# Kernel tuning notes

Measured on AMD Instinct MI355X. Metric: run time of the kernel, lower is better.

The kernel has to match this reference:

```python
import jax, jax.numpy as jnp
import numpy as np

NUM_EMBEDDINGS = 1024
EMBEDDING_DIM = 64


def setup_inputs() -> dict:
    key = jax.random.key(0)
    k1, k2 = jax.random.split(key)
    x = jax.random.normal(k1, (32, 64, 32, 32), dtype=jnp.float32)
    # embeddings initialized uniform(-1/K, 1/K) as in the torch module
    codebook = jax.random.uniform(
        k2, (NUM_EMBEDDINGS, EMBEDDING_DIM), dtype=jnp.float32,
        minval=-1.0 / NUM_EMBEDDINGS, maxval=1.0 / NUM_EMBEDDINGS)
    return {"x": x, "codebook": codebook}


def reference(x, codebook):
    # x: [B, D, H, W] -> [B, H, W, D]
    xp = jnp.transpose(x, (0, 2, 3, 1))
    B, H, W, D = xp.shape
    K = codebook.shape[0]
    xf = xp.reshape(-1, D)  # [N, D]
    # squared L2 distances via expansion (argmin identical to torch.norm argmin)
    x2 = jnp.sum(xf * xf, axis=1, keepdims=True)          # [N, 1]
    c2 = jnp.sum(codebook * codebook, axis=1)             # [K]
    d2 = x2 - 2.0 * (xf @ codebook.T) + c2[None, :]       # [N, K]
    idx = jnp.argmin(d2, axis=1)                          # [N]
    encodings = jax.nn.one_hot(idx, K, dtype=jnp.float32)  # [N, K]
    quantized = codebook[idx]                             # [N, D] == encodings @ codebook
    quantized = quantized.reshape(B, H, W, D).transpose(0, 3, 1, 2)
    return encodings, quantized
```

## Files before the change

kernel.cpp:

```cpp
#include <hip/hip_runtime.h>

#define N_PIX    32768
#define DIM      64
#define K_CODES  1024
#define NCHUNK   4
#define CHUNK    256
#define BPIX     128
#define CS_STR   260


__global__ __launch_bounds__(256) void c2_kernel(const float* __restrict__ cb,
                                                 float* __restrict__ c2) {
    int k = blockIdx.x * 256 + threadIdx.x;
    if (k >= K_CODES) return;
    const float* row = cb + k * DIM;
    float a0 = 0.f, a1 = 0.f, a2 = 0.f, a3 = 0.f;
#pragma unroll
    for (int d = 0; d < DIM; d += 4) {
        a0 = fmaf(row[d + 0], row[d + 0], a0);
        a1 = fmaf(row[d + 1], row[d + 1], a1);
        a2 = fmaf(row[d + 2], row[d + 2], a2);
        a3 = fmaf(row[d + 3], row[d + 3], a3);
    }
    c2[k] = (a0 + a1) + (a2 + a3);
}

__global__ __launch_bounds__(512, 2) void argmin_tile(const float* __restrict__ x,
                                                      const float* __restrict__ cb,
                                                      const float* __restrict__ c2,
                                                      int* __restrict__ idx,
                                                      float* __restrict__ quant) {
    __shared__ alignas(16) float xs[DIM * BPIX];
    __shared__ alignas(16) float cs[DIM * CS_STR];
    __shared__ float  xn[BPIX];
    __shared__ float2 red[4][BPIX];

    const int t      = threadIdx.x;
    const int blk    = blockIdx.x;
    const int p_base = blk * BPIX;
    const int bb     = p_base >> 10;
    const int hw0    = p_base & 1023;

    const float4* x4  = reinterpret_cast<const float4*>(x);
    const float4* cb4 = reinterpret_cast<const float4*>(cb);

#pragma unroll
    for (int i = 0; i < 4; ++i) {
        int fidx = i * 512 + t;
        int d = fidx >> 5, p4 = fidx & 31;
        float4 v = x4[(size_t)bb * 16384 + (size_t)d * 256 + (hw0 >> 2) + p4];
        *reinterpret_cast<float4*>(&xs[d * BPIX + p4 * 4]) = v;
    }
    __syncthreads();

    if (t < BPIX) {
        float s0 = 0.f, s1 = 0.f, s2 = 0.f, s3 = 0.f;
#pragma unroll
        for (int d = 0; d < DIM; d += 4) {
            float v0 = xs[(d + 0) * BPIX + t];
            float v1 = xs[(d + 1) * BPIX + t];
            float v2 = xs[(d + 2) * BPIX + t];
            float v3 = xs[(d + 3) * BPIX + t];
            s0 = fmaf(v0, v0, s0);
            s1 = fmaf(v1, v1, s1);
            s2 = fmaf(v2, v2, s2);
            s3 = fmaf(v3, v3, s3);
        }
        xn[t] = (s0 + s1) + (s2 + s3);
    }

    const int lane = t & 63, w = t >> 6;
    const int wy = lane >> 3, wx = lane & 7;
    const int wr = w >> 2,    wc = w & 3;
    const int pl0 = wr * 64 + wy * 8;
    const int kl0 = wc * 64 + wx * 8;

    float bv[8]; int bk[8]; float xnr[8];
#pragma unroll
    for (int i = 0; i < 8; ++i) { bv[i] = 1e30f; bk[i] = 0; }

    float4 creg[8];
#pragma unroll
    for (int i = 0; i < 8; ++i) {
        int fidx = i * 512 + t; int k = fidx & 255, dq = fidx >> 8;
        creg[i] = cb4[(size_t)k * 16 + dq];
    }
    __syncthreads();

#pragma unroll
    for (int i = 0; i < 8; ++i) xnr[i] = xn[pl0 + i];

    for (int c = 0; c < NCHUNK; ++c) {
#pragma unroll
        for (int i = 0; i < 8; ++i) {
            int fidx = i * 512 + t; int k = fidx & 255, dq = fidx >> 8;
            cs[(4 * dq + 0) * CS_STR + k] = creg[i].x;
            cs[(4 * dq + 1) * CS_STR + k] = creg[i].y;
            cs[(4 * dq + 2) * CS_STR + k] = creg[i].z;
            cs[(4 * dq + 3) * CS_STR + k] = creg[i].w;
        }
        if (c + 1 < NCHUNK) {
#pragma unroll
            for (int i = 0; i < 8; ++i) {
                int fidx = i * 512 + t; int k = fidx & 255, dq = fidx >> 8;
                creg[i] = cb4[(size_t)((c + 1) * CHUNK + k) * 16 + dq];
            }
        }
        __syncthreads();

        float acc[8][8];
#pragma unroll
        for (int i = 0; i < 8; ++i)
#pragma unroll
            for (int j = 0; j < 8; ++j) acc[i][j] = 0.f;

#pragma unroll 4
        for (int d = 0; d < DIM; ++d) {
            const float* xr = &xs[d * BPIX + pl0];
            const float* cr = &cs[d * CS_STR + kl0];
            float4 xlo = *reinterpret_cast<const float4*>(xr);
            float4 xhi = *reinterpret_cast<const float4*>(xr + 4);
            float4 clo = *reinterpret_cast<const float4*>(cr);
            float4 chi = *reinterpret_cast<const float4*>(cr + 4);
#define ROW(i, xi) \
            acc[i][0] = fmaf(xi, clo.x, acc[i][0]); \
            acc[i][1] = fmaf(xi, clo.y, acc[i][1]); \
            acc[i][2] = fmaf(xi, clo.z, acc[i][2]); \
            acc[i][3] = fmaf(xi, clo.w, acc[i][3]); \
            acc[i][4] = fmaf(xi, chi.x, acc[i][4]); \
            acc[i][5] = fmaf(xi, chi.y, acc[i][5]); \
            acc[i][6] = fmaf(xi, chi.z, acc[i][6]); \
            acc[i][7] = fmaf(xi, chi.w, acc[i][7]);
            ROW(0, xlo.x) ROW(1, xlo.y) ROW(2, xlo.z) ROW(3, xlo.w)
            ROW(4, xhi.x) ROW(5, xhi.y) ROW(6, xhi.z) ROW(7, xhi.w)
#undef ROW
        }

        float4 c2lo = *reinterpret_cast<const float4*>(&c2[c * CHUNK + kl0]);
        float4 c2hi = *reinterpret_cast<const float4*>(&c2[c * CHUNK + kl0 + 4]);
        float c2a[8] = {c2lo.x, c2lo.y, c2lo.z, c2lo.w, c2hi.x, c2hi.y, c2hi.z, c2hi.w};
#pragma unroll
        for (int i = 0; i < 8; ++i) {
#pragma unroll
            for (int j = 0; j < 8; ++j) {
                int   k    = c * CHUNK + kl0 + j;
                float u    = xnr[i] - 2.0f * acc[i][j];
                float dist = u + c2a[j];
                if (dist < bv[i]) { bv[i] = dist; bk[i] = k; }
            }
        }
        __syncthreads();
    }

#pragma unroll
    for (int i = 0; i < 8; ++i) {
#pragma unroll
        for (int off = 1; off <= 4; off <<= 1) {
            float ov = __shfl_xor(bv[i], off);
            int   ok = __shfl_xor(bk[i], off);
            if (ov < bv[i] || (ov == bv[i] && ok < bk[i])) { bv[i] = ov; bk[i] = ok; }
        }
    }
    if (wx == 0) {
#pragma unroll
        for (int i = 0; i < 8; ++i)
            red[wc][pl0 + i] = make_float2(bv[i], __int_as_float(bk[i]));
    }
    __syncthreads();

    if (t < BPIX) {
        float fv = 1e30f; int fk = 0;
#pragma unroll
        for (int cc = 0; cc < 4; ++cc) {
            float2 r  = red[cc][t];
            int    rk = __float_as_int(r.y);
            if (r.x < fv || (r.x == fv && rk < fk)) { fv = r.x; fk = rk; }
        }
        idx[p_base + t] = fk;

        const float4* crow = cb4 + (size_t)fk * 16;
        float* qb = quant + (size_t)bb * (DIM * 1024) + (hw0 + t);
#pragma unroll
        for (int dq = 0; dq < 16; ++dq) {
            float4 cv = crow[dq];
            qb[(size_t)(dq * 4 + 0) << 10] = cv.x;
            qb[(size_t)(dq * 4 + 1) << 10] = cv.y;
            qb[(size_t)(dq * 4 + 2) << 10] = cv.z;
            qb[(size_t)(dq * 4 + 3) << 10] = cv.w;
        }
    }
}

__global__ __launch_bounds__(256) void enc_write(const int* __restrict__ idx,
                                                 float* __restrict__ enc) {
    const int TOT = (N_PIX / 4) * K_CODES;
    int tid = blockIdx.x * 256 + threadIdx.x;
    float4* enc4 = reinterpret_cast<float4*>(enc);
    for (int e = tid; e < TOT; e += 2048 * 256) {
        int n  = e >> 8;
        int j0 = (e & 255) << 2;
        int ir = idx[n];
        float4 v;
        v.x = (ir == j0 + 0) ? 1.0f : 0.0f;
        v.y = (ir == j0 + 1) ? 1.0f : 0.0f;
        v.z = (ir == j0 + 2) ? 1.0f : 0.0f;
        v.w = (ir == j0 + 3) ? 1.0f : 0.0f;
        enc4[e] = v;
    }
}

extern "C" void kernel_launch(void* const* d_in, const int* in_sizes, int n_in,
                              void* d_out, int out_size, void* d_ws, size_t ws_size,
                              hipStream_t stream) {
    const float* x  = (const float*)d_in[0];
    const float* cb = (const float*)d_in[1];

    float* c2  = (float*)d_ws;
    int*   idx = (int*)((char*)d_ws + 4096);

    float* enc   = (float*)d_out;
    float* quant = (float*)d_out + (size_t)N_PIX * K_CODES;

    c2_kernel<<<K_CODES / 256, 256, 0, stream>>>(cb, c2);
    argmin_tile<<<N_PIX / BPIX, 512, 0, stream>>>(x, cb, c2, idx, quant);
    enc_write<<<2048, 256, 0, stream>>>(idx, enc);
}
```

Before: 208.9 us.

## Split codebook across blocks with larger pixel tiles and separate reduce kernel

The argmin kernel now handles 256 pixels per block, and each block covers only half of the codebook, so the grid has 256 blocks. Each thread computes an 8x16 register tile instead of 8x8 to raise the ratio of FMAs to LDS reads. The unpadded codebook tile is read at strided float4 offsets. A new reduce_quant kernel merges the two half-codebook partial minima and writes the idx and quantized outputs. The trade-offs are higher register pressure from the 128 accumulators, an extra kernel launch, and a round trip through global memory for the partial results.

```diff
diff --git a/kernel.cpp b/kernel.cpp
--- a/kernel.cpp
+++ b/kernel.cpp
@@ -3,10 +3,9 @@
 #define N_PIX    32768
 #define DIM      64
 #define K_CODES  1024
-#define NCHUNK   4
+#define BPIX     256
 #define CHUNK    256
-#define BPIX     128
-#define CS_STR   260
+#define NSPLIT   2
 
 
 __global__ __launch_bounds__(256) void c2_kernel(const float* __restrict__ cb,
@@ -28,28 +27,37 @@
 __global__ __launch_bounds__(512, 2) void argmin_tile(const float* __restrict__ x,
                                                       const float* __restrict__ cb,
                                                       const float* __restrict__ c2,
-                                                      int* __restrict__ idx,
-                                                      float* __restrict__ quant) {
+                                                      float2* __restrict__ part) {
     __shared__ alignas(16) float xs[DIM * BPIX];
-    __shared__ alignas(16) float cs[DIM * CS_STR];
+    __shared__ alignas(16) float cs[DIM * CHUNK];
     __shared__ float  xn[BPIX];
-    __shared__ float2 red[4][BPIX];
+    __shared__ float2 red[2][BPIX];
 
     const int t      = threadIdx.x;
     const int blk    = blockIdx.x;
-    const int p_base = blk * BPIX;
+    const int ks     = blk & 1;
+    const int pixblk = blk >> 1;
+    const int p_base = pixblk * BPIX;
     const int bb     = p_base >> 10;
     const int hw0    = p_base & 1023;
 
     const float4* x4  = reinterpret_cast<const float4*>(x);
     const float4* cb4 = reinterpret_cast<const float4*>(cb);
 
-#pragma unroll
-    for (int i = 0; i < 4; ++i) {
+    float4 creg[8];
+#pragma unroll
+    for (int i = 0; i < 8; ++i) {
         int fidx = i * 512 + t;
-        int d = fidx >> 5, p4 = fidx & 31;
-        float4 v = x4[(size_t)bb * 16384 + (size_t)d * 256 + (hw0 >> 2) + p4];
-        *reinterpret_cast<float4*>(&xs[d * BPIX + p4 * 4]) = v;
+        int k = fidx & 255, dq = fidx >> 8;
+        creg[i] = cb4[(size_t)(ks * 512 + k) * 16 + dq];
+    }
+
+#pragma unroll
+    for (int i = 0; i < 8; ++i) {
+        int fidx = i * 512 + t;
+        int d = fidx >> 6, p4 = fidx & 63;
+        reinterpret_cast<float4*>(xs)[d * 64 + p4] =
+            x4[(size_t)bb * 16384 + (size_t)d * 256 + (hw0 >> 2) + p4];
     }
     __syncthreads();
 
@@ -71,82 +79,86 @@
 
     const int lane = t & 63, w = t >> 6;
     const int wy = lane >> 3, wx = lane & 7;
-    const int wr = w >> 2,    wc = w & 3;
+    const int wr = w >> 1,    wc = w & 1;
     const int pl0 = wr * 64 + wy * 8;
-    const int kl0 = wc * 64 + wx * 8;
+    const int kb  = wc * 128;
+    const int wx4 = wx * 4;
 
     float bv[8]; int bk[8]; float xnr[8];
 #pragma unroll
     for (int i = 0; i < 8; ++i) { bv[i] = 1e30f; bk[i] = 0; }
 
-    float4 creg[8];
-#pragma unroll
-    for (int i = 0; i < 8; ++i) {
-        int fidx = i * 512 + t; int k = fidx & 255, dq = fidx >> 8;
-        creg[i] = cb4[(size_t)k * 16 + dq];
-    }
-    __syncthreads();
-
-#pragma unroll
-    for (int i = 0; i < 8; ++i) xnr[i] = xn[pl0 + i];
-
-    for (int c = 0; c < NCHUNK; ++c) {
+    float acc[8][16];
+
+    for (int ch = 0; ch < 2; ++ch) {
 #pragma unroll
         for (int i = 0; i < 8; ++i) {
-            int fidx = i * 512 + t; int k = fidx & 255, dq = fidx >> 8;
-            cs[(4 * dq + 0) * CS_STR + k] = creg[i].x;
-            cs[(4 * dq + 1) * CS_STR + k] = creg[i].y;
-            cs[(4 * dq + 2) * CS_STR + k] = creg[i].z;
-            cs[(4 * dq + 3) * CS_STR + k] = creg[i].w;
-        }
-        if (c + 1 < NCHUNK) {
+            int fidx = i * 512 + t;
+            int k = fidx & 255, dq = fidx >> 8;
+            cs[(4 * dq + 0) * CHUNK + k] = creg[i].x;
+            cs[(4 * dq + 1) * CHUNK + k] = creg[i].y;
+            cs[(4 * dq + 2) * CHUNK + k] = creg[i].z;
+            cs[(4 * dq + 3) * CHUNK + k] = creg[i].w;
+        }
+        if (ch == 0) {
 #pragma unroll
             for (int i = 0; i < 8; ++i) {
-                int fidx = i * 512 + t; int k = fidx & 255, dq = fidx >> 8;
-                creg[i] = cb4[(size_t)((c + 1) * CHUNK + k) * 16 + dq];
+                int fidx = i * 512 + t;
+                int k = fidx & 255, dq = fidx >> 8;
+                creg[i] = cb4[(size_t)(ks * 512 + 256 + k) * 16 + dq];
             }
         }
         __syncthreads();
 
-        float acc[8][8];
+        if (ch == 0) {
+#pragma unroll
+            for (int i = 0; i < 8; ++i) xnr[i] = xn[pl0 + i];
+        }
+
 #pragma unroll
         for (int i = 0; i < 8; ++i)
 #pragma unroll
-            for (int j = 0; j < 8; ++j) acc[i][j] = 0.f;
-
-#pragma unroll 4
+            for (int j = 0; j < 16; ++j) acc[i][j] = 0.f;
+
+#pragma unroll 2
         for (int d = 0; d < DIM; ++d) {
-            const float* xr = &xs[d * BPIX + pl0];
-            const float* cr = &cs[d * CS_STR + kl0];
+            const float* xr = xs + d * BPIX + pl0;
+            const float* cr = cs + d * CHUNK + kb + wx4;
             float4 xlo = *reinterpret_cast<const float4*>(xr);
             float4 xhi = *reinterpret_cast<const float4*>(xr + 4);
-            float4 clo = *reinterpret_cast<const float4*>(cr);
-            float4 chi = *reinterpret_cast<const float4*>(cr + 4);
+            float4 cfA = *reinterpret_cast<const float4*>(cr);
+            float4 cfB = *reinterpret_cast<const float4*>(cr + 32);
+            float4 cfC = *reinterpret_cast<const float4*>(cr + 64);
+            float4 cfD = *reinterpret_cast<const float4*>(cr + 96);
 #define ROW(i, xi) \
-            acc[i][0] = fmaf(xi, clo.x, acc[i][0]); \
-            acc[i][1] = fmaf(xi, clo.y, acc[i][1]); \
-            acc[i][2] = fmaf(xi, clo.z, acc[i][2]); \
-            acc[i][3] = fmaf(xi, clo.w, acc[i][3]); \
-            acc[i][4] = fmaf(xi, chi.x, acc[i][4]); \
-            acc[i][5] = fmaf(xi, chi.y, acc[i][5]); \
-            acc[i][6] = fmaf(xi, chi.z, acc[i][6]); \
-            acc[i][7] = fmaf(xi, chi.w, acc[i][7]);
+            acc[i][ 0]=fmaf(xi,cfA.x,acc[i][ 0]); acc[i][ 1]=fmaf(xi,cfA.y,acc[i][ 1]); \
+            acc[i][ 2]=fmaf(xi,cfA.z,acc[i][ 2]); acc[i][ 3]=fmaf(xi,cfA.w,acc[i][ 3]); \
+            acc[i][ 4]=fmaf(xi,cfB.x,acc[i][ 4]); acc[i][ 5]=fmaf(xi,cfB.y,acc[i][ 5]); \
+            acc[i][ 6]=fmaf(xi,cfB.z,acc[i][ 6]); acc[i][ 7]=fmaf(xi,cfB.w,acc[i][ 7]); \
+            acc[i][ 8]=fmaf(xi,cfC.x,acc[i][ 8]); acc[i][ 9]=fmaf(xi,cfC.y,acc[i][ 9]); \
+            acc[i][10]=fmaf(xi,cfC.z,acc[i][10]); acc[i][11]=fmaf(xi,cfC.w,acc[i][11]); \
+            acc[i][12]=fmaf(xi,cfD.x,acc[i][12]); acc[i][13]=fmaf(xi,cfD.y,acc[i][13]); \
+            acc[i][14]=fmaf(xi,cfD.z,acc[i][14]); acc[i][15]=fmaf(xi,cfD.w,acc[i][15]);
             ROW(0, xlo.x) ROW(1, xlo.y) ROW(2, xlo.z) ROW(3, xlo.w)
             ROW(4, xhi.x) ROW(5, xhi.y) ROW(6, xhi.z) ROW(7, xhi.w)
 #undef ROW
         }
 
-        float4 c2lo = *reinterpret_cast<const float4*>(&c2[c * CHUNK + kl0]);
-        float4 c2hi = *reinterpret_cast<const float4*>(&c2[c * CHUNK + kl0 + 4]);
-        float c2a[8] = {c2lo.x, c2lo.y, c2lo.z, c2lo.w, c2hi.x, c2hi.y, c2hi.z, c2hi.w};
-#pragma unroll
-        for (int i = 0; i < 8; ++i) {
-#pragma unroll
-            for (int j = 0; j < 8; ++j) {
-                int   k    = c * CHUNK + kl0 + j;
-                float u    = xnr[i] - 2.0f * acc[i][j];
-                float dist = u + c2a[j];
-                if (dist < bv[i]) { bv[i] = dist; bk[i] = k; }
+        int kgc = ks * 512 + ch * 256 + kb + wx4;
+#pragma unroll
+        for (int j = 0; j < 4; ++j) {
+            float4 c2v = *reinterpret_cast<const float4*>(&c2[kgc + j * 32]);
+#pragma unroll
+            for (int i = 0; i < 8; ++i) {
+                float d0 = (xnr[i] - 2.0f * acc[i][j * 4 + 0]) + c2v.x;
+                float d1 = (xnr[i] - 2.0f * acc[i][j * 4 + 1]) + c2v.y;
+                float d2 = (xnr[i] - 2.0f * acc[i][j * 4 + 2]) + c2v.z;
+                float d3 = (xnr[i] - 2.0f * acc[i][j * 4 + 3]) + c2v.w;
+                int k = kgc + j * 32;
+                if (d0 < bv[i]) { bv[i] = d0; bk[i] = k + 0; }
+                if (d1 < bv[i]) { bv[i] = d1; bk[i] = k + 1; }
+                if (d2 < bv[i]) { bv[i] = d2; bk[i] = k + 2; }
+                if (d3 < bv[i]) { bv[i] = d3; bk[i] = k + 3; }
             }
         }
         __syncthreads();
@@ -169,25 +181,36 @@
     __syncthreads();
 
     if (t < BPIX) {
-        float fv = 1e30f; int fk = 0;
-#pragma unroll
-        for (int cc = 0; cc < 4; ++cc) {
-            float2 r  = red[cc][t];
-            int    rk = __float_as_int(r.y);
-            if (r.x < fv || (r.x == fv && rk < fk)) { fv = r.x; fk = rk; }
-        }
-        idx[p_base + t] = fk;
-
-        const float4* crow = cb4 + (size_t)fk * 16;
-        float* qb = quant + (size_t)bb * (DIM * 1024) + (hw0 + t);
-#pragma unroll
-        for (int dq = 0; dq < 16; ++dq) {
-            float4 cv = crow[dq];
-            qb[(size_t)(dq * 4 + 0) << 10] = cv.x;
-            qb[(size_t)(dq * 4 + 1) << 10] = cv.y;
-            qb[(size_t)(dq * 4 + 2) << 10] = cv.z;
-            qb[(size_t)(dq * 4 + 3) << 10] = cv.w;
-        }
+        float2 r0 = red[0][t], r1 = red[1][t];
+        int k0i = __float_as_int(r0.y), k1i = __float_as_int(r1.y);
+        float fv = r0.x; int fk = k0i;
+        if (r1.x < fv || (r1.x == fv && k1i < fk)) { fv = r1.x; fk = k1i; }
+        part[(size_t)ks * N_PIX + p_base + t] = make_float2(fv, __int_as_float(fk));
+    }
+}
+
+__global__ __launch_bounds__(128) void reduce_quant(const float* __restrict__ cb,
+                                                    const float2* __restrict__ part,
+                                                    int* __restrict__ idx,
+                                                    float* __restrict__ quant) {
+    int n = blockIdx.x * 128 + threadIdx.x;
+    float2 r0 = part[n];
+    float2 r1 = part[(size_t)N_PIX + n];
+    float best = r0.x; int bi = __float_as_int(r0.y);
+    if (r1.x < best) { best = r1.x; bi = __float_as_int(r1.y); }
+    idx[n] = bi;
+
+    int bb = n >> 10;
+    int hw = n & 1023;
+    const float4* crow = reinterpret_cast<const float4*>(cb + (size_t)bi * DIM);
+    float* qb = quant + (size_t)bb * (DIM * 1024) + hw;
+#pragma unroll
+    for (int dq = 0; dq < 16; ++dq) {
+        float4 cv = crow[dq];
+        qb[(size_t)(dq * 4 + 0) << 10] = cv.x;
+        qb[(size_t)(dq * 4 + 1) << 10] = cv.y;
+        qb[(size_t)(dq * 4 + 2) << 10] = cv.z;
+        qb[(size_t)(dq * 4 + 3) << 10] = cv.w;
     }
 }
 
@@ -215,13 +238,15 @@
     const float* x  = (const float*)d_in[0];
     const float* cb = (const float*)d_in[1];
 
-    float* c2  = (float*)d_ws;
-    int*   idx = (int*)((char*)d_ws + 4096);
+    float*  c2   = (float*)d_ws;
+    float2* part = (float2*)((char*)d_ws + 4096);
+    int*    idx  = (int*)((char*)d_ws + 4096 + (size_t)NSPLIT * N_PIX * 8);
 
     float* enc   = (float*)d_out;
     float* quant = (float*)d_out + (size_t)N_PIX * K_CODES;
 
     c2_kernel<<<K_CODES / 256, 256, 0, stream>>>(cb, c2);
-    argmin_tile<<<N_PIX / BPIX, 512, 0, stream>>>(x, cb, c2, idx, quant);
+    argmin_tile<<<(N_PIX / BPIX) * NSPLIT, 512, 0, stream>>>(x, cb, c2, part);
+    reduce_quant<<<N_PIX / 128, 128, 0, stream>>>(cb, part, idx, quant);
     enc_write<<<2048, 256, 0, stream>>>(idx, enc);
 }
```

Result: slower. 248.6 us (+19.0%).

## Split codebook across blocks and reduce argmin partials in separate kernel

Applied to the files above, without the earlier changes.

The argmin kernel no longer has each block loop over all 1024 codes. It now launches eight blocks per 128-pixel tile, each scoring one 128-code slice with 256 threads and writing partial (distance, index) pairs to workspace. A new reduce kernel picks the final index per pixel and writes the quantized output. This raises grid parallelism from 256 to 2048 blocks to fill the GPU's CUs, at the cost of reloading x eight times, an extra kernel launch, and partial-result traffic through global memory.

```diff
diff --git a/kernel.cpp b/kernel.cpp
--- a/kernel.cpp
+++ b/kernel.cpp
@@ -3,10 +3,9 @@
 #define N_PIX    32768
 #define DIM      64
 #define K_CODES  1024
-#define NCHUNK   4
-#define CHUNK    256
 #define BPIX     128
-#define CS_STR   260
+#define CHUNK    128
+#define NSPLIT   8
 
 
 __global__ __launch_bounds__(256) void c2_kernel(const float* __restrict__ cb,
@@ -25,31 +24,53 @@
     c2[k] = (a0 + a1) + (a2 + a3);
 }
 
-__global__ __launch_bounds__(512, 2) void argmin_tile(const float* __restrict__ x,
+__global__ __launch_bounds__(256, 4) void argmin_tile(const float* __restrict__ x,
                                                       const float* __restrict__ cb,
                                                       const float* __restrict__ c2,
-                                                      int* __restrict__ idx,
-                                                      float* __restrict__ quant) {
+                                                      float2* __restrict__ part) {
     __shared__ alignas(16) float xs[DIM * BPIX];
-    __shared__ alignas(16) float cs[DIM * CS_STR];
+    __shared__ alignas(16) float cs[DIM * CHUNK];
     __shared__ float  xn[BPIX];
-    __shared__ float2 red[4][BPIX];
+    __shared__ float2 red[2][BPIX];
 
     const int t      = threadIdx.x;
     const int blk    = blockIdx.x;
-    const int p_base = blk * BPIX;
+    const int split  = blk & 7;
+    const int pixblk = blk >> 3;
+    const int p_base = pixblk * BPIX;
     const int bb     = p_base >> 10;
     const int hw0    = p_base & 1023;
+    const int k_base = split * CHUNK;
 
     const float4* x4  = reinterpret_cast<const float4*>(x);
     const float4* cb4 = reinterpret_cast<const float4*>(cb);
 
 #pragma unroll
-    for (int i = 0; i < 4; ++i) {
-        int fidx = i * 512 + t;
+    for (int i = 0; i < 8; ++i) {
+        int fidx = i * 256 + t;
         int d = fidx >> 5, p4 = fidx & 31;
-        float4 v = x4[(size_t)bb * 16384 + (size_t)d * 256 + (hw0 >> 2) + p4];
-        *reinterpret_cast<float4*>(&xs[d * BPIX + p4 * 4]) = v;
+        reinterpret_cast<float4*>(xs)[d * 32 + p4] =
+            x4[(size_t)bb * 16384 + (size_t)d * 256 + (hw0 >> 2) + p4];
+    }
+
+#pragma unroll
+    for (int pass = 0; pass < 2; ++pass) {
+        float4 creg[4];
+#pragma unroll
+        for (int i = 0; i < 4; ++i) {
+            int fidx = pass * 1024 + i * 256 + t;
+            int k = fidx & 127, dq = fidx >> 7;
+            creg[i] = cb4[(size_t)(k_base + k) * 16 + dq];
+        }
+#pragma unroll
+        for (int i = 0; i < 4; ++i) {
+            int fidx = pass * 1024 + i * 256 + t;
+            int k = fidx & 127, dq = fidx >> 7;
+            cs[(4 * dq + 0) * CHUNK + k] = creg[i].x;
+            cs[(4 * dq + 1) * CHUNK + k] = creg[i].y;
+            cs[(4 * dq + 2) * CHUNK + k] = creg[i].z;
+            cs[(4 * dq + 3) * CHUNK + k] = creg[i].w;
+        }
     }
     __syncthreads();
 
@@ -71,85 +92,55 @@
 
     const int lane = t & 63, w = t >> 6;
     const int wy = lane >> 3, wx = lane & 7;
-    const int wr = w >> 2,    wc = w & 3;
+    const int wr = w >> 1,    wc = w & 1;
     const int pl0 = wr * 64 + wy * 8;
     const int kl0 = wc * 64 + wx * 8;
 
-    float bv[8]; int bk[8]; float xnr[8];
-#pragma unroll
-    for (int i = 0; i < 8; ++i) { bv[i] = 1e30f; bk[i] = 0; }
-
-    float4 creg[8];
-#pragma unroll
-    for (int i = 0; i < 8; ++i) {
-        int fidx = i * 512 + t; int k = fidx & 255, dq = fidx >> 8;
-        creg[i] = cb4[(size_t)k * 16 + dq];
+    float acc[8][8];
+#pragma unroll
+    for (int i = 0; i < 8; ++i)
+#pragma unroll
+        for (int j = 0; j < 8; ++j) acc[i][j] = 0.f;
+
+#pragma unroll 2
+    for (int d = 0; d < DIM; ++d) {
+        const float* xr = xs + d * BPIX + pl0;
+        const float* cr = cs + d * CHUNK + kl0;
+        float4 xlo = *reinterpret_cast<const float4*>(xr);
+        float4 xhi = *reinterpret_cast<const float4*>(xr + 4);
+        float4 clo = *reinterpret_cast<const float4*>(cr);
+        float4 chi = *reinterpret_cast<const float4*>(cr + 4);
+#define ROW(i, xi) \
+        acc[i][0] = fmaf(xi, clo.x, acc[i][0]); \
+        acc[i][1] = fmaf(xi, clo.y, acc[i][1]); \
+        acc[i][2] = fmaf(xi, clo.z, acc[i][2]); \
+        acc[i][3] = fmaf(xi, clo.w, acc[i][3]); \
+        acc[i][4] = fmaf(xi, chi.x, acc[i][4]); \
+        acc[i][5] = fmaf(xi, chi.y, acc[i][5]); \
+        acc[i][6] = fmaf(xi, chi.z, acc[i][6]); \
+        acc[i][7] = fmaf(xi, chi.w, acc[i][7]);
+        ROW(0, xlo.x) ROW(1, xlo.y) ROW(2, xlo.z) ROW(3, xlo.w)
+        ROW(4, xhi.x) ROW(5, xhi.y) ROW(6, xhi.z) ROW(7, xhi.w)
+#undef ROW
     }
     __syncthreads();
 
-#pragma unroll
-    for (int i = 0; i < 8; ++i) xnr[i] = xn[pl0 + i];
-
-    for (int c = 0; c < NCHUNK; ++c) {
+    float bv[8]; int bk[8];
+    {
+        float4 c2lo = *reinterpret_cast<const float4*>(&c2[k_base + kl0]);
+        float4 c2hi = *reinterpret_cast<const float4*>(&c2[k_base + kl0 + 4]);
+        float c2a[8] = {c2lo.x, c2lo.y, c2lo.z, c2lo.w,
+                        c2hi.x, c2hi.y, c2hi.z, c2hi.w};
 #pragma unroll
         for (int i = 0; i < 8; ++i) {
-            int fidx = i * 512 + t; int k = fidx & 255, dq = fidx >> 8;
-            cs[(4 * dq + 0) * CS_STR + k] = creg[i].x;
-            cs[(4 * dq + 1) * CS_STR + k] = creg[i].y;
-            cs[(4 * dq + 2) * CS_STR + k] = creg[i].z;
-            cs[(4 * dq + 3) * CS_STR + k] = creg[i].w;
-        }
-        if (c + 1 < NCHUNK) {
-#pragma unroll
-            for (int i = 0; i < 8; ++i) {
-                int fidx = i * 512 + t; int k = fidx & 255, dq = fidx >> 8;
-                creg[i] = cb4[(size_t)((c + 1) * CHUNK + k) * 16 + dq];
+            float xni = xn[pl0 + i];
+            bv[i] = 1e30f; bk[i] = 0;
+#pragma unroll
+            for (int j = 0; j < 8; ++j) {
+                float dist = (xni - 2.0f * acc[i][j]) + c2a[j];
+                if (dist < bv[i]) { bv[i] = dist; bk[i] = k_base + kl0 + j; }
             }
         }
-        __syncthreads();
-
-        float acc[8][8];
-#pragma unroll
-        for (int i = 0; i < 8; ++i)
-#pragma unroll
-            for (int j = 0; j < 8; ++j) acc[i][j] = 0.f;
-
-#pragma unroll 4
-        for (int d = 0; d < DIM; ++d) {
-            const float* xr = &xs[d * BPIX + pl0];
-            const float* cr = &cs[d * CS_STR + kl0];
-            float4 xlo = *reinterpret_cast<const float4*>(xr);
-            float4 xhi = *reinterpret_cast<const float4*>(xr + 4);
-            float4 clo = *reinterpret_cast<const float4*>(cr);
-            float4 chi = *reinterpret_cast<const float4*>(cr + 4);
-#define ROW(i, xi) \
-            acc[i][0] = fmaf(xi, clo.x, acc[i][0]); \
-            acc[i][1] = fmaf(xi, clo.y, acc[i][1]); \
-            acc[i][2] = fmaf(xi, clo.z, acc[i][2]); \
-            acc[i][3] = fmaf(xi, clo.w, acc[i][3]); \
-            acc[i][4] = fmaf(xi, chi.x, acc[i][4]); \
-            acc[i][5] = fmaf(xi, chi.y, acc[i][5]); \
-            acc[i][6] = fmaf(xi, chi.z, acc[i][6]); \
-            acc[i][7] = fmaf(xi, chi.w, acc[i][7]);
-            ROW(0, xlo.x) ROW(1, xlo.y) ROW(2, xlo.z) ROW(3, xlo.w)
-            ROW(4, xhi.x) ROW(5, xhi.y) ROW(6, xhi.z) ROW(7, xhi.w)
-#undef ROW
-        }
-
-        float4 c2lo = *reinterpret_cast<const float4*>(&c2[c * CHUNK + kl0]);
-        float4 c2hi = *reinterpret_cast<const float4*>(&c2[c * CHUNK + kl0 + 4]);
-        float c2a[8] = {c2lo.x, c2lo.y, c2lo.z, c2lo.w, c2hi.x, c2hi.y, c2hi.z, c2hi.w};
-#pragma unroll
-        for (int i = 0; i < 8; ++i) {
-#pragma unroll
-            for (int j = 0; j < 8; ++j) {
-                int   k    = c * CHUNK + kl0 + j;
-                float u    = xnr[i] - 2.0f * acc[i][j];
-                float dist = u + c2a[j];
-                if (dist < bv[i]) { bv[i] = dist; bk[i] = k; }
-            }
-        }
-        __syncthreads();
     }
 
 #pragma unroll
@@ -169,25 +160,39 @@
     __syncthreads();
 
     if (t < BPIX) {
-        float fv = 1e30f; int fk = 0;
-#pragma unroll
-        for (int cc = 0; cc < 4; ++cc) {
-            float2 r  = red[cc][t];
-            int    rk = __float_as_int(r.y);
-            if (r.x < fv || (r.x == fv && rk < fk)) { fv = r.x; fk = rk; }
-        }
-        idx[p_base + t] = fk;
-
-        const float4* crow = cb4 + (size_t)fk * 16;
-        float* qb = quant + (size_t)bb * (DIM * 1024) + (hw0 + t);
-#pragma unroll
-        for (int dq = 0; dq < 16; ++dq) {
-            float4 cv = crow[dq];
-            qb[(size_t)(dq * 4 + 0) << 10] = cv.x;
-            qb[(size_t)(dq * 4 + 1) << 10] = cv.y;
-            qb[(size_t)(dq * 4 + 2) << 10] = cv.z;
-            qb[(size_t)(dq * 4 + 3) << 10] = cv.w;
-        }
+        float2 r0 = red[0][t], r1 = red[1][t];
+        int k0i = __float_as_int(r0.y), k1i = __float_as_int(r1.y);
+        float fv = r0.x; int fk = k0i;
+        if (r1.x < fv || (r1.x == fv && k1i < fk)) { fv = r1.x; fk = k1i; }
+        part[(size_t)split * N_PIX + p_base + t] = make_float2(fv, __int_as_float(fk));
+    }
+}
+
+__global__ __launch_bounds__(128) void reduce_quant(const float* __restrict__ cb,
+                                                    const float2* __restrict__ part,
+                                                    int* __restrict__ idx,
+                                                    float* __restrict__ quant) {
+    int n = blockIdx.x * 128 + threadIdx.x;
+    float best = 1e30f;
+    int   bi = 0;
+#pragma unroll
+    for (int c = 0; c < NSPLIT; ++c) {
+        float2 r = part[(size_t)c * N_PIX + n];
+        if (r.x < best) { best = r.x; bi = __float_as_int(r.y); }
+    }
+    idx[n] = bi;
+
+    int bb = n >> 10;
+    int hw = n & 1023;
+    const float4* crow = reinterpret_cast<const float4*>(cb + (size_t)bi * DIM);
+    float* qb = quant + (size_t)bb * (DIM * 1024) + hw;
+#pragma unroll
+    for (int dq = 0; dq < 16; ++dq) {
+        float4 cv = crow[dq];
+        qb[(size_t)(dq * 4 + 0) << 10] = cv.x;
+        qb[(size_t)(dq * 4 + 1) << 10] = cv.y;
+        qb[(size_t)(dq * 4 + 2) << 10] = cv.z;
+        qb[(size_t)(dq * 4 + 3) << 10] = cv.w;
     }
 }
 
@@ -215,13 +220,15 @@
     const float* x  = (const float*)d_in[0];
     const float* cb = (const float*)d_in[1];
 
-    float* c2  = (float*)d_ws;
-    int*   idx = (int*)((char*)d_ws + 4096);
+    float*  c2   = (float*)d_ws;
+    float2* part = (float2*)((char*)d_ws + 4096);
+    int*    idx  = (int*)((char*)d_ws + 4096 + (size_t)NSPLIT * N_PIX * 8);
 
     float* enc   = (float*)d_out;
     float* quant = (float*)d_out + (size_t)N_PIX * K_CODES;
 
     c2_kernel<<<K_CODES / 256, 256, 0, stream>>>(cb, c2);
-    argmin_tile<<<N_PIX / BPIX, 512, 0, stream>>>(x, cb, c2, idx, quant);
+    argmin_tile<<<(N_PIX / BPIX) * NSPLIT, 256, 0, stream>>>(x, cb, c2, part);
+    reduce_quant<<<N_PIX / 128, 128, 0, stream>>>(cb, part, idx, quant);
     enc_write<<<2048, 256, 0, stream>>>(idx, enc);
 }
```

Measured after the change: 228.6 us. 1.09x slower.

## Drop codebook smem padding, interleave code columns, spread quantized write over all threads

Applied to the files above, without the earlier changes.

The codebook shared tile loses its padded stride (260 becomes 256). Each thread now reads two float4 groups 32 floats apart instead of 8 contiguous values, which changes the shared-memory bank access pattern of the inner product loop. The first codebook chunk's global load is hoisted alongside the x tile load so both share one barrier. The quantized-output gather now uses all 512 threads (each handles a quarter of the dimensions) instead of 128. This adds an extra barrier and shared index array, and the unpadded stores into the codebook tile may hit bank conflicts.

```diff
diff --git a/kernel.cpp b/kernel.cpp
--- a/kernel.cpp
+++ b/kernel.cpp
@@ -3,10 +3,9 @@
 #define N_PIX    32768
 #define DIM      64
 #define K_CODES  1024
+#define BPIX     128
+#define CHUNK    256
 #define NCHUNK   4
-#define CHUNK    256
-#define BPIX     128
-#define CS_STR   260
 
 
 __global__ __launch_bounds__(256) void c2_kernel(const float* __restrict__ cb,
@@ -31,9 +30,10 @@
                                                       int* __restrict__ idx,
                                                       float* __restrict__ quant) {
     __shared__ alignas(16) float xs[DIM * BPIX];
-    __shared__ alignas(16) float cs[DIM * CS_STR];
+    __shared__ alignas(16) float cs[DIM * CHUNK];
     __shared__ float  xn[BPIX];
     __shared__ float2 red[4][BPIX];
+    __shared__ int    sidx[BPIX];
 
     const int t      = threadIdx.x;
     const int blk    = blockIdx.x;
@@ -48,8 +48,16 @@
     for (int i = 0; i < 4; ++i) {
         int fidx = i * 512 + t;
         int d = fidx >> 5, p4 = fidx & 31;
-        float4 v = x4[(size_t)bb * 16384 + (size_t)d * 256 + (hw0 >> 2) + p4];
-        *reinterpret_cast<float4*>(&xs[d * BPIX + p4 * 4]) = v;
+        reinterpret_cast<float4*>(xs)[d * 32 + p4] =
+            x4[(size_t)bb * 16384 + (size_t)d * 256 + (hw0 >> 2) + p4];
+    }
+
+    float4 creg[8];
+#pragma unroll
+    for (int i = 0; i < 8; ++i) {
+        int fidx = i * 512 + t;
+        int k = fidx & 255, dq = fidx >> 8;
+        creg[i] = cb4[(size_t)k * 16 + dq];
     }
     __syncthreads();
 
@@ -73,40 +81,36 @@
     const int wy = lane >> 3, wx = lane & 7;
     const int wr = w >> 2,    wc = w & 3;
     const int pl0 = wr * 64 + wy * 8;
-    const int kl0 = wc * 64 + wx * 8;
+    const int kc0 = wc * 64 + wx * 4;
 
     float bv[8]; int bk[8]; float xnr[8];
 #pragma unroll
     for (int i = 0; i < 8; ++i) { bv[i] = 1e30f; bk[i] = 0; }
 
-    float4 creg[8];
-#pragma unroll
-    for (int i = 0; i < 8; ++i) {
-        int fidx = i * 512 + t; int k = fidx & 255, dq = fidx >> 8;
-        creg[i] = cb4[(size_t)k * 16 + dq];
-    }
-    __syncthreads();
-
-#pragma unroll
-    for (int i = 0; i < 8; ++i) xnr[i] = xn[pl0 + i];
-
-    for (int c = 0; c < NCHUNK; ++c) {
+    for (int ch = 0; ch < NCHUNK; ++ch) {
 #pragma unroll
         for (int i = 0; i < 8; ++i) {
-            int fidx = i * 512 + t; int k = fidx & 255, dq = fidx >> 8;
-            cs[(4 * dq + 0) * CS_STR + k] = creg[i].x;
-            cs[(4 * dq + 1) * CS_STR + k] = creg[i].y;
-            cs[(4 * dq + 2) * CS_STR + k] = creg[i].z;
-            cs[(4 * dq + 3) * CS_STR + k] = creg[i].w;
-        }
-        if (c + 1 < NCHUNK) {
+            int fidx = i * 512 + t;
+            int k = fidx & 255, dq = fidx >> 8;
+            cs[(4 * dq + 0) * CHUNK + k] = creg[i].x;
+            cs[(4 * dq + 1) * CHUNK + k] = creg[i].y;
+            cs[(4 * dq + 2) * CHUNK + k] = creg[i].z;
+            cs[(4 * dq + 3) * CHUNK + k] = creg[i].w;
+        }
+        if (ch + 1 < NCHUNK) {
 #pragma unroll
             for (int i = 0; i < 8; ++i) {
-                int fidx = i * 512 + t; int k = fidx & 255, dq = fidx >> 8;
-                creg[i] = cb4[(size_t)((c + 1) * CHUNK + k) * 16 + dq];
+                int fidx = i * 512 + t;
+                int k = fidx & 255, dq = fidx >> 8;
+                creg[i] = cb4[(size_t)((ch + 1) * CHUNK + k) * 16 + dq];
             }
         }
         __syncthreads();
+
+        if (ch == 0) {
+#pragma unroll
+            for (int i = 0; i < 8; ++i) xnr[i] = xn[pl0 + i];
+        }
 
         float acc[8][8];
 #pragma unroll
@@ -116,36 +120,36 @@
 
 #pragma unroll 4
         for (int d = 0; d < DIM; ++d) {
-            const float* xr = &xs[d * BPIX + pl0];
-            const float* cr = &cs[d * CS_STR + kl0];
+            const float* xr = xs + d * BPIX + pl0;
+            const float* cr = cs + d * CHUNK + kc0;
             float4 xlo = *reinterpret_cast<const float4*>(xr);
             float4 xhi = *reinterpret_cast<const float4*>(xr + 4);
-            float4 clo = *reinterpret_cast<const float4*>(cr);
-            float4 chi = *reinterpret_cast<const float4*>(cr + 4);
+            float4 cfA = *reinterpret_cast<const float4*>(cr);
+            float4 cfB = *reinterpret_cast<const float4*>(cr + 32);
 #define ROW(i, xi) \
-            acc[i][0] = fmaf(xi, clo.x, acc[i][0]); \
-            acc[i][1] = fmaf(xi, clo.y, acc[i][1]); \
-            acc[i][2] = fmaf(xi, clo.z, acc[i][2]); \
-            acc[i][3] = fmaf(xi, clo.w, acc[i][3]); \
-            acc[i][4] = fmaf(xi, chi.x, acc[i][4]); \
-            acc[i][5] = fmaf(xi, chi.y, acc[i][5]); \
-            acc[i][6] = fmaf(xi, chi.z, acc[i][6]); \
-            acc[i][7] = fmaf(xi, chi.w, acc[i][7]);
+            acc[i][0] = fmaf(xi, cfA.x, acc[i][0]); \
+            acc[i][1] = fmaf(xi, cfA.y, acc[i][1]); \
+            acc[i][2] = fmaf(xi, cfA.z, acc[i][2]); \
+            acc[i][3] = fmaf(xi, cfA.w, acc[i][3]); \
+            acc[i][4] = fmaf(xi, cfB.x, acc[i][4]); \
+            acc[i][5] = fmaf(xi, cfB.y, acc[i][5]); \
+            acc[i][6] = fmaf(xi, cfB.z, acc[i][6]); \
+            acc[i][7] = fmaf(xi, cfB.w, acc[i][7]);
             ROW(0, xlo.x) ROW(1, xlo.y) ROW(2, xlo.z) ROW(3, xlo.w)
             ROW(4, xhi.x) ROW(5, xhi.y) ROW(6, xhi.z) ROW(7, xhi.w)
 #undef ROW
         }
 
-        float4 c2lo = *reinterpret_cast<const float4*>(&c2[c * CHUNK + kl0]);
-        float4 c2hi = *reinterpret_cast<const float4*>(&c2[c * CHUNK + kl0 + 4]);
-        float c2a[8] = {c2lo.x, c2lo.y, c2lo.z, c2lo.w, c2hi.x, c2hi.y, c2hi.z, c2hi.w};
+        int kg = ch * CHUNK + kc0;
+        float4 c2A = *reinterpret_cast<const float4*>(&c2[kg]);
+        float4 c2B = *reinterpret_cast<const float4*>(&c2[kg + 32]);
+        float c2a[8] = {c2A.x, c2A.y, c2A.z, c2A.w, c2B.x, c2B.y, c2B.z, c2B.w};
 #pragma unroll
         for (int i = 0; i < 8; ++i) {
 #pragma unroll
             for (int j = 0; j < 8; ++j) {
-                int   k    = c * CHUNK + kl0 + j;
-                float u    = xnr[i] - 2.0f * acc[i][j];
-                float dist = u + c2a[j];
+                float dist = (xnr[i] - 2.0f * acc[i][j]) + c2a[j];
+                int   k    = kg + (j >> 2) * 32 + (j & 3);
                 if (dist < bv[i]) { bv[i] = dist; bk[i] = k; }
             }
         }
@@ -176,12 +180,19 @@
             int    rk = __float_as_int(r.y);
             if (r.x < fv || (r.x == fv && rk < fk)) { fv = r.x; fk = rk; }
         }
+        sidx[t] = fk;
         idx[p_base + t] = fk;
-
-        const float4* crow = cb4 + (size_t)fk * 16;
-        float* qb = quant + (size_t)bb * (DIM * 1024) + (hw0 + t);
-#pragma unroll
-        for (int dq = 0; dq < 16; ++dq) {
+    }
+    __syncthreads();
+
+    {
+        int r = t & 127, q = t >> 7;
+        int fk = sidx[r];
+        const float4* crow = cb4 + (size_t)fk * 16 + q * 4;
+        float* qb = quant + (size_t)bb * (DIM * 1024) + (size_t)(q * 16) * 1024
+                    + (hw0 + r);
+#pragma unroll
+        for (int dq = 0; dq < 4; ++dq) {
             float4 cv = crow[dq];
             qb[(size_t)(dq * 4 + 0) << 10] = cv.x;
             qb[(size_t)(dq * 4 + 1) << 10] = cv.y;
```

Result: no change. 208.0 us (-0.5%).
